# Kernel tuning notes

Measured on AMD Instinct MI355X. Metric: run time of the kernel, lower is better.

The kernel has to match this reference:

```python
import jax, jax.numpy as jnp
import numpy as np
from jax import lax

NUM_IM, ROIS = 32, 128          # images per batch, proposals per image
NUM_CLASSES, EMBED, OBJ_DIM = 151, 200, 2048
HALF_H = 256                    # per-direction LSTM hidden; bi concat -> 512
BN_EPS = 1e-5


def _lstm_dir(xs, wih, whh, b):
    # xs: [T, B, Din] -> hidden states [T, B, H]
    pre = jnp.einsum('tbd,dh->tbh', xs, wih) + b  # precompute input proj
    H = whh.shape[0]
    h0 = jnp.zeros((xs.shape[1], H), xs.dtype)
    def step(carry, pt):
        h, c = carry
        g = pt + h @ whh
        i, f, gg, o = jnp.split(g, 4, axis=-1)
        c = jax.nn.sigmoid(f) * c + jax.nn.sigmoid(i) * jnp.tanh(gg)
        h = jax.nn.sigmoid(o) * jnp.tanh(c)
        return (h, c), h
    _, hs = lax.scan(step, (h0, h0), pre)
    return hs


def _bilstm(x, wih, whh, b):
    # x: [B, T, D] -> [B, T, 2*HALF_H]; wih/whh/b carry both directions on axis 0
    xs = jnp.swapaxes(x, 0, 1)
    fwd = _lstm_dir(xs, wih[0], whh[0], b[0])
    bwd = _lstm_dir(xs[::-1], wih[1], whh[1], b[1])[::-1]
    return jnp.swapaxes(jnp.concatenate([fwd, bwd], -1), 0, 1)


def _context(feats, conf, params):
    # sort_rois: per-image descending confidence order, run 2-layer bi(tree)LSTM,
    # then scatter back with the inverse permutation (as in _sort_by_score).
    D = feats.shape[-1]
    f = feats.reshape(NUM_IM, ROIS, D)
    perm = jnp.argsort(-conf.reshape(NUM_IM, ROIS), axis=1)
    xs = jnp.take_along_axis(f, perm[..., None], axis=1)
    wih0, whh0, b0, wih1, whh1, b1 = params
    h = _bilstm(xs, wih0, whh0, b0)
    h = _bilstm(h, wih1, whh1, b1)
    inv = jnp.argsort(perm, axis=1)
    h = jnp.take_along_axis(h, inv[..., None], axis=1)
    return h.reshape(NUM_IM * ROIS, -1)


def setup_inputs() -> dict:
    key = jax.random.key(0)
    ks = jax.random.split(key, 24)
    N = NUM_IM * ROIS
    obj_fmaps = jax.random.normal(ks[0], (N, OBJ_DIM), jnp.float32)
    obj_logits = jax.random.normal(ks[1], (N, NUM_CLASSES), jnp.float32)
    xy = jax.random.uniform(ks[2], (N, 2), jnp.float32) * 500.0
    wh = jax.random.uniform(ks[3], (N, 2), jnp.float32) * 100.0 + 1.0
    boxes = jnp.concatenate([xy, xy + wh], axis=1)  # valid x1y1x2y2
    im_inds = jnp.repeat(jnp.arange(NUM_IM, dtype=jnp.int64), ROIS)
    w = lambda k, s: (jax.random.normal(k, s, jnp.float32) * 0.02)
    H4 = 4 * HALF_H
    D_obj, D_edge = OBJ_DIM + EMBED + 128, EMBED + 2 * HALF_H + OBJ_DIM
    return {
        'obj_fmaps': obj_fmaps, 'obj_logits': obj_logits, 'boxes': boxes,
        'im_inds': im_inds,
        'obj_embed_w': w(ks[4], (NUM_CLASSES, EMBED)),
        'obj_embed2_w': w(ks[5], (NUM_CLASSES, EMBED)),
        'bn_gamma': jnp.ones((4,), jnp.float32), 'bn_beta': jnp.zeros((4,), jnp.float32),
        'bn_mean': jnp.zeros((4,), jnp.float32), 'bn_var': jnp.ones((4,), jnp.float32),
        'pos_w': w(ks[6], (4, 128)), 'pos_b': jnp.zeros((128,), jnp.float32),
        'obj_wih0': w(ks[7], (2, D_obj, H4)), 'obj_whh0': w(ks[8], (2, HALF_H, H4)),
        'obj_b0': jnp.zeros((2, H4), jnp.float32),
        'obj_wih1': w(ks[9], (2, 2 * HALF_H, H4)), 'obj_whh1': w(ks[10], (2, HALF_H, H4)),
        'obj_b1': jnp.zeros((2, H4), jnp.float32),
        'edge_wih0': w(ks[11], (2, D_edge, H4)), 'edge_whh0': w(ks[12], (2, HALF_H, H4)),
        'edge_b0': jnp.zeros((2, H4), jnp.float32),
        'edge_wih1': w(ks[13], (2, 2 * HALF_H, H4)), 'edge_whh1': w(ks[14], (2, HALF_H, H4)),
        'edge_b1': jnp.zeros((2, H4), jnp.float32),
        'dec_w': w(ks[15], (D_obj + 2 * HALF_H, NUM_CLASSES)),
        'dec_b': jnp.zeros((NUM_CLASSES,), jnp.float32),
    }


def reference(obj_fmaps, obj_logits, boxes, im_inds, obj_embed_w, obj_embed2_w,
              bn_gamma, bn_beta, bn_mean, bn_var, pos_w, pos_b,
              obj_wih0, obj_whh0, obj_b0, obj_wih1, obj_whh1, obj_b1,
              edge_wih0, edge_whh0, edge_b0, edge_wih1, edge_whh1, edge_b1,
              dec_w, dec_b):
    probs = jax.nn.softmax(obj_logits, axis=-1)
    obj_embed = probs @ obj_embed_w                      # soft class embedding
    x1, y1, x2, y2 = boxes[:, 0], boxes[:, 1], boxes[:, 2], boxes[:, 3]
    cs = jnp.stack([(x1 + x2) * 0.5, (y1 + y2) * 0.5, x2 - x1, y2 - y1], axis=-1)
    csn = (cs - bn_mean) * lax.rsqrt(bn_var + BN_EPS) * bn_gamma + bn_beta
    pos = jax.nn.relu(csn @ pos_w + pos_b)               # BN(4)+Linear(4,128)+ReLU
    feats = jnp.concatenate([obj_fmaps, obj_embed, pos], axis=-1)  # [N, 2376]
    conf = jnp.max(probs[:, 1:], axis=-1)                # confidence (non-bg)
    enc = _context(feats, conf, (obj_wih0, obj_whh0, obj_b0,
                                 obj_wih1, obj_whh1, obj_b1))       # [N, 512]
    dec_in = jnp.concatenate([feats, enc], axis=-1)      # pass_in_obj_feats_to_decoder
    obj_dists = dec_in @ dec_w + dec_b                   # [N, 151]
    obj_preds = jnp.argmax(obj_dists[:, 1:], axis=-1) + 1
    edge_in = jnp.concatenate([obj_embed2_w[obj_preds], enc, obj_fmaps], axis=-1)
    edge_ctx = _context(edge_in, conf, (edge_wih0, edge_whh0, edge_b0,
                                        edge_wih1, edge_whh1, edge_b1))  # [N, 512]
    return jnp.concatenate([obj_dists, edge_ctx], axis=-1)  # [N, 663]
```

## Files before the change

kernel.cpp:

```cpp
#include <hip/hip_runtime.h>
#include <hip/hip_bf16.h>
#include <hip/hip_fp16.h>

typedef unsigned short u16;
typedef unsigned int u32;
typedef short s16x8 __attribute__((ext_vector_type(8)));
typedef float f32x4 __attribute__((ext_vector_type(4)));

#define FE_LD 2944
#define EDGE_LD 2816

static __device__ __forceinline__ int sdot4(u32 a, u32 b, int acc) {
  return __builtin_amdgcn_sdot4((int)a, (int)b, acc, false);
}
static __device__ __forceinline__ float fsig(float x) {
  return __builtin_amdgcn_rcpf(1.f + __expf(-x));
}
static __device__ __forceinline__ float ftanh(float x) {
  return 1.f - 2.f * __builtin_amdgcn_rcpf(1.f + __expf(2.f * x));
}

#define GLD_LDS16(gsrc, ldst) \
  __builtin_amdgcn_global_load_lds((const __attribute__((address_space(1))) void*)(gsrc), \
                                   (__attribute__((address_space(3))) void*)(ldst), 16, 0, 0)

__global__ __launch_bounds__(256) void gemm_kernel(
    const u16* __restrict__ A, int lda,
    const u16* __restrict__ B, int ldb,
    int K, int N,
    float* __restrict__ outF, __hip_bfloat16* __restrict__ outB, int ldc,
    const float* __restrict__ bias)
{
  __shared__ __align__(16) u16 As[128*64];
  __shared__ __align__(16) u16 Bs[128*64];
  const int tid = threadIdx.x;
  const int w = tid >> 6, lane = tid & 63;
  const int wm = w >> 1, wn = w & 1;
  const long bm = (long)blockIdx.x * 128;
  const long bn = (long)blockIdx.y * 128;
  f32x4 acc[4][4] = {};

  for (int k0 = 0; k0 < K; k0 += 64) {
    #pragma unroll
    for (int rr = 0; rr < 4; rr++) {
      int idx = rr * 256 + tid;
      int row = idx >> 3;
      int g   = idx & 7;
      int gs  = g ^ (row & 7);
      int ldst = (rr * 256 + (w << 6)) * 8;
      GLD_LDS16(A + (bm + row) * (long)lda + k0 + gs * 8, &As[ldst]);
      GLD_LDS16(B + (bn + row) * (long)ldb + k0 + gs * 8, &Bs[ldst]);
    }
    __syncthreads();
    #pragma unroll
    for (int kk = 0; kk < 2; kk++) {
      s16x8 af[4], bfr[4];
      #pragma unroll
      for (int i = 0; i < 4; i++) {
        int ra = wm * 64 + i * 16 + (lane & 15);
        int rb = wn * 64 + i * 16 + (lane & 15);
        int gg = kk * 4 + (lane >> 4);
        af[i]  = *(const s16x8*)&As[ra * 64 + ((gg ^ (ra & 7)) << 3)];
        bfr[i] = *(const s16x8*)&Bs[rb * 64 + ((gg ^ (rb & 7)) << 3)];
      }
      #pragma unroll
      for (int i = 0; i < 4; i++)
        #pragma unroll
        for (int j = 0; j < 4; j++)
          acc[i][j] = __builtin_amdgcn_mfma_f32_16x16x32_bf16(af[i], bfr[j], acc[i][j], 0, 0, 0);
    }
    __syncthreads();
  }

  #pragma unroll
  for (int i = 0; i < 4; i++)
    #pragma unroll
    for (int j = 0; j < 4; j++)
      #pragma unroll
      for (int v = 0; v < 4; v++) {
        long rr = bm + wm * 64 + i * 16 + (lane >> 4) * 4 + v;
        int  cc = (int)bn + wn * 64 + j * 16 + (lane & 15);
        if (cc < N) {
          float val = acc[i][j][v] + (bias ? bias[cc] : 0.f);
          if (outF) outF[rr * (long)ldc + cc] = val;
          else      outB[rr * (long)ldc + cc] = __float2bfloat16(val);
        }
      }
}

#define N_TROPS 10
struct TrOps {
  const float* src[N_TROPS];
  __hip_bfloat16* dst[N_TROPS];
  int srcK[N_TROPS], srcN[N_TROPS], dstR[N_TROPS], dstC[N_TROPS];
  int split[N_TROPS], soff[N_TROPS];
  int tileBase[N_TROPS], tilesX[N_TROPS];
};
__global__ void transpose_batch(TrOps ops)
{
  __shared__ float tile[32][33];
  int bid = blockIdx.x;
  int op = 0;
  #pragma unroll
  for (int i = 1; i < N_TROPS; i++) if (bid >= ops.tileBase[i]) op = i;
  const int local = bid - ops.tileBase[op];
  const int kt = (local % ops.tilesX[op]) * 32;
  const int nt = (local / ops.tilesX[op]) * 32;
  const float* src = ops.src[op];
  __hip_bfloat16* dst = ops.dst[op];
  const int srcK = ops.srcK[op], srcN = ops.srcN[op];
  const int dstR = ops.dstR[op], dstC = ops.dstC[op];
  const int split = ops.split[op], soff = ops.soff[op];

  const int tx = threadIdx.x & 31, ty = threadIdx.x >> 5;
  for (int i = ty; i < 32; i += 8) {
    int k = kt + i;
    int srck = (k < split) ? (soff + k) : (k - split);
    int n = nt + tx;
    tile[i][tx] = (srck < srcK && n < srcN) ? src[(size_t)srck * srcN + n] : 0.f;
  }
  __syncthreads();
  for (int i = ty; i < 32; i += 8) {
    int n = nt + i, k = kt + tx;
    if (n < dstR && k < dstC)
      dst[(size_t)n * dstC + k] = __float2bfloat16(tile[tx][i]);
  }
}

struct PkOps {
  const float* whh[4];
  u32* wreg[4];
  u32* wlds[4];
  float* wsc[4];
};
__global__ void pack_batch(PkOps ops)
{
  const int set = blockIdx.y;
  const float* whh = ops.whh[set];
  u32* wreg = ops.wreg[set];
  u32* wlds = ops.wlds[set];
  float* wsc = ops.wsc[set];

  const int idx = blockIdx.x * 256 + threadIdx.x;
  const int d = idx >> 10, col = idx & 1023;
  const int c4 = col >> 8, j = col & 255;
  const float* s = whh + (size_t)d * 256 * 1024 + col;
  float mx = 0.f;
  for (int k = 0; k < 256; k++) mx = fmaxf(mx, fabsf(s[(size_t)k * 1024]));
  float inv = (mx > 0.f) ? 127.f / mx : 0.f;
  wsc[d * 1024 + col] = (mx > 0.f) ? mx / (127.f * 127.f) : 0.f;
  const int rc = (c4 < 2) ? 12 : 8;
  const int rb = (c4 == 0) ? 0 : (c4 == 1) ? 12 : (c4 == 2) ? 24 : 32;
  for (int kg = 0; kg < 4; kg++) {
    const int slot = kg * 256 + j;
    for (int w = 0; w < 16; w++) {
      u32 v = 0;
      #pragma unroll
      for (int b = 0; b < 4; b++) {
        int q = __float2int_rn(s[(size_t)(kg * 64 + 4 * w + b) * 1024] * inv);
        q = max(-127, min(127, q));
        v |= ((u32)(q & 0xff)) << (8 * b);
      }
      if (w < rc) {
        wreg[(size_t)(d * 40 + rb + w) * 1024 + slot] = v;
      } else {
        int qq, comp;
        if (c4 == 0)      { qq = 0; comp = w - 12; }
        else if (c4 == 1) { qq = 1; comp = w - 12; }
        else if (c4 == 2) { qq = 2 + ((w - 8) >> 2); comp = (w - 8) & 3; }
        else              { qq = 4 + ((w - 8) >> 2); comp = (w - 8) & 3; }
        wlds[((size_t)(d * 6 + qq) * 1024 + slot) * 4 + comp] = v;
      }
    }
  }
}

__global__ void prep_kernel(
    const float* __restrict__ logits, const float* __restrict__ fmaps,
    const float* __restrict__ boxes,
    const float* __restrict__ bn_g, const float* __restrict__ bn_b,
    const float* __restrict__ bn_m, const float* __restrict__ bn_v,
    const float* __restrict__ pos_w, const float* __restrict__ pos_b,
    __hip_bfloat16* __restrict__ FE, __hip_bfloat16* __restrict__ probsb,
    float* __restrict__ conf)
{
  __shared__ float red[256];
  const int row = blockIdx.x, t = threadIdx.x;
  float v = (t < 151) ? logits[(size_t)row * 151 + t] : -3.0e38f;
  red[t] = v; __syncthreads();
  for (int s = 128; s > 0; s >>= 1) { if (t < s) red[t] = fmaxf(red[t], red[t + s]); __syncthreads(); }
  float mx = red[0]; __syncthreads();
  float p = (t < 151) ? expf(v - mx) : 0.f;
  red[t] = p; __syncthreads();
  for (int s = 128; s > 0; s >>= 1) { if (t < s) red[t] += red[t + s]; __syncthreads(); }
  float sum = red[0]; __syncthreads();
  p = p / sum;
  if (t < 192) probsb[(size_t)row * 192 + t] = __float2bfloat16((t < 151) ? p : 0.f);
  red[t] = (t >= 1 && t < 151) ? p : 0.f; __syncthreads();
  for (int s = 128; s > 0; s >>= 1) { if (t < s) red[t] = fmaxf(red[t], red[t + s]); __syncthreads(); }
  if (t == 0) conf[row] = red[0];

  if (t < 128) {
    float x1 = boxes[row * 4 + 0], y1 = boxes[row * 4 + 1];
    float x2 = boxes[row * 4 + 2], y2 = boxes[row * 4 + 3];
    float cs[4] = { (x1 + x2) * 0.5f, (y1 + y2) * 0.5f, x2 - x1, y2 - y1 };
    float a = pos_b[t];
    #pragma unroll
    for (int j = 0; j < 4; j++) {
      float cn = (cs[j] - bn_m[j]) * rsqrtf(bn_v[j] + 1e-5f) * bn_g[j] + bn_b[j];
      a += cn * pos_w[j * 128 + t];
    }
    FE[(size_t)row * FE_LD + 2760 + t] = __float2bfloat16(fmaxf(a, 0.f));
  }
  for (int c0 = t; c0 < 2048; c0 += 256)
    FE[(size_t)row * FE_LD + 512 + c0] = __float2bfloat16(fmaps[(size_t)row * 2048 + c0]);
}

__global__ void sort_kernel(const float* __restrict__ conf, int* __restrict__ perm)
{
  __shared__ float key[128];
  __shared__ int   idx[128];
  const int b = blockIdx.x, t = threadIdx.x;
  key[t] = conf[b * 128 + t]; idx[t] = t;
  __syncthreads();
  for (int k = 2; k <= 128; k <<= 1)
    for (int j = k >> 1; j > 0; j >>= 1) {
      int ixj = t ^ j;
      if (ixj > t) {
        bool up = (t & k) == 0;
        float ka = key[t], kb = key[ixj];
        int ia = idx[t], ib = idx[ixj];
        bool before = (ka > kb) || (ka == kb && ia < ib);
        if (before != up) { key[t] = kb; key[ixj] = ka; idx[t] = ib; idx[ixj] = ia; }
      }
      __syncthreads();
    }
  perm[b * 128 + t] = b * 128 + idx[t];
}

__global__ __launch_bounds__(1024) void rec_kernel(
    const __hip_bfloat16* __restrict__ P,
    const int* __restrict__ perm,
    const u32* __restrict__ wreg_g,
    const uint4* __restrict__ wlds_g,
    const float* __restrict__ wsc_g,
    int gatherPerm, int outPerm,
    __hip_bfloat16* __restrict__ out_bf, int out_ld,
    float* __restrict__ out_f32, int f32_ld, int f32_off)
{
  __shared__ __align__(16) uint4 wt4[6 * 1024];
  __shared__ __align__(16) int4 part[256 * 5];
  __shared__ __align__(16) u32 hq[64];
  __shared__ int prow_lds[128];
  const int tid = threadIdx.x;
  const int kg = tid >> 8;
  const int img = blockIdx.x & 31, dir = blockIdx.x >> 5;

  u32 wv[40];
  {
    const u32* rp = wreg_g + (size_t)dir * 40960 + tid;
    #pragma unroll
    for (int i = 0; i < 40; i++) wv[i] = rp[(size_t)i * 1024];
  }
  #pragma unroll
  for (int i = 0; i < 40; i++) asm volatile("" : "+v"(wv[i]));
  {
    const uint4* lp = wlds_g + (size_t)dir * 6144 + tid;
    #pragma unroll
    for (int q = 0; q < 6; q++) wt4[q * 1024 + tid] = lp[(size_t)q * 1024];
  }
  if (tid < 128) prow_lds[tid] = perm[img * 128 + tid];
  if (tid < 64) hq[tid] = 0;

  float sc0 = 0.f, sc1 = 0.f, sc2 = 0.f, sc3 = 0.f, cst = 0.f;
  if (tid < 256) {
    const float* sp = wsc_g + dir * 1024 + tid;
    sc0 = sp[0]; sc1 = sp[256]; sc2 = sp[512]; sc3 = sp[768];
  }
  __syncthreads();

  const uint4* hq4 = (const uint4*)hq;

  int st = dir ? 127 : 0;
  float p0 = 0.f, p1 = 0.f, p2 = 0.f, p3 = 0.f;
  if (tid < 256) {
    int prow0 = gatherPerm ? prow_lds[st] : (img * 128 + st);
    const __hip_bfloat16* pp = P + (size_t)prow0 * 2048 + dir * 1024 + tid;
    p0 = __bfloat162float(pp[0]);   p1 = __bfloat162float(pp[256]);
    p2 = __bfloat162float(pp[512]); p3 = __bfloat162float(pp[768]);
  }

  for (int t = 0; t < 128; t++) {
    float n0 = 0.f, n1 = 0.f, n2 = 0.f, n3 = 0.f;
    if (tid < 256 && t < 127) {
      int stn = dir ? (126 - t) : (t + 1);
      int prn = gatherPerm ? prow_lds[stn] : (img * 128 + stn);
      const __hip_bfloat16* pp = P + (size_t)prn * 2048 + dir * 1024 + tid;
      n0 = __bfloat162float(pp[0]);   n1 = __bfloat162float(pp[256]);
      n2 = __bfloat162float(pp[512]); n3 = __bfloat162float(pp[768]);
    }

    int a0 = 0, a1 = 0, a2 = 0, a3 = 0;
    {
      uint4 hv = hq4[kg * 4 + 0];
      a0 = sdot4(hv.x, wv[0], a0);  a0 = sdot4(hv.y, wv[1], a0);
      a0 = sdot4(hv.z, wv[2], a0);  a0 = sdot4(hv.w, wv[3], a0);
      a1 = sdot4(hv.x, wv[12], a1); a1 = sdot4(hv.y, wv[13], a1);
      a1 = sdot4(hv.z, wv[14], a1); a1 = sdot4(hv.w, wv[15], a1);
      a2 = sdot4(hv.x, wv[24], a2); a2 = sdot4(hv.y, wv[25], a2);
      a2 = sdot4(hv.z, wv[26], a2); a2 = sdot4(hv.w, wv[27], a2);
      a3 = sdot4(hv.x, wv[32], a3); a3 = sdot4(hv.y, wv[33], a3);
      a3 = sdot4(hv.z, wv[34], a3); a3 = sdot4(hv.w, wv[35], a3);
    }
    {
      uint4 hv = hq4[kg * 4 + 1];
      a0 = sdot4(hv.x, wv[4], a0);  a0 = sdot4(hv.y, wv[5], a0);
      a0 = sdot4(hv.z, wv[6], a0);  a0 = sdot4(hv.w, wv[7], a0);
      a1 = sdot4(hv.x, wv[16], a1); a1 = sdot4(hv.y, wv[17], a1);
      a1 = sdot4(hv.z, wv[18], a1); a1 = sdot4(hv.w, wv[19], a1);
      a2 = sdot4(hv.x, wv[28], a2); a2 = sdot4(hv.y, wv[29], a2);
      a2 = sdot4(hv.z, wv[30], a2); a2 = sdot4(hv.w, wv[31], a2);
      a3 = sdot4(hv.x, wv[36], a3); a3 = sdot4(hv.y, wv[37], a3);
      a3 = sdot4(hv.z, wv[38], a3); a3 = sdot4(hv.w, wv[39], a3);
    }
    {
      uint4 hv = hq4[kg * 4 + 2];
      a0 = sdot4(hv.x, wv[8], a0);  a0 = sdot4(hv.y, wv[9], a0);
      a0 = sdot4(hv.z, wv[10], a0); a0 = sdot4(hv.w, wv[11], a0);
      a1 = sdot4(hv.x, wv[20], a1); a1 = sdot4(hv.y, wv[21], a1);
      a1 = sdot4(hv.z, wv[22], a1); a1 = sdot4(hv.w, wv[23], a1);
      uint4 wl = wt4[2 * 1024 + tid];
      a2 = sdot4(hv.x, wl.x, a2); a2 = sdot4(hv.y, wl.y, a2);
      a2 = sdot4(hv.z, wl.z, a2); a2 = sdot4(hv.w, wl.w, a2);
      wl = wt4[4 * 1024 + tid];
      a3 = sdot4(hv.x, wl.x, a3); a3 = sdot4(hv.y, wl.y, a3);
      a3 = sdot4(hv.z, wl.z, a3); a3 = sdot4(hv.w, wl.w, a3);
    }
    {
      uint4 hv = hq4[kg * 4 + 3];
      uint4 wl = wt4[0 * 1024 + tid];
      a0 = sdot4(hv.x, wl.x, a0); a0 = sdot4(hv.y, wl.y, a0);
      a0 = sdot4(hv.z, wl.z, a0); a0 = sdot4(hv.w, wl.w, a0);
      wl = wt4[1 * 1024 + tid];
      a1 = sdot4(hv.x, wl.x, a1); a1 = sdot4(hv.y, wl.y, a1);
      a1 = sdot4(hv.z, wl.z, a1); a1 = sdot4(hv.w, wl.w, a1);
      wl = wt4[3 * 1024 + tid];
      a2 = sdot4(hv.x, wl.x, a2); a2 = sdot4(hv.y, wl.y, a2);
      a2 = sdot4(hv.z, wl.z, a2); a2 = sdot4(hv.w, wl.w, a2);
      wl = wt4[5 * 1024 + tid];
      a3 = sdot4(hv.x, wl.x, a3); a3 = sdot4(hv.y, wl.y, a3);
      a3 = sdot4(hv.z, wl.z, a3); a3 = sdot4(hv.w, wl.w, a3);
    }

    part[(tid & 255) * 5 + kg] = int4{a0, a1, a2, a3};
    __syncthreads();

    if (tid < 256) {
      int4 q0 = part[tid * 5 + 0], q1 = part[tid * 5 + 1];
      int4 q2 = part[tid * 5 + 2], q3 = part[tid * 5 + 3];
      float gi = (float)(q0.x + q1.x + q2.x + q3.x) * sc0 + p0;
      float gf = (float)(q0.y + q1.y + q2.y + q3.y) * sc1 + p1;
      float gg = (float)(q0.z + q1.z + q2.z + q3.z) * sc2 + p2;
      float go = (float)(q0.w + q1.w + q2.w + q3.w) * sc3 + p3;
      float si = fsig(gi), sf = fsig(gf), so = fsig(go);
      cst = sf * cst + si * ftanh(gg);
      float h = so * ftanh(cst);
      int qi = __float2int_rn(h * 127.f);
      ((signed char*)hq)[tid] = (signed char)qi;
      const int orow = outPerm ? prow_lds[st] : (img * 128 + st);
      if (out_bf)  out_bf[(size_t)orow * out_ld + dir * 256 + tid] = __float2bfloat16(h);
      if (out_f32) out_f32[(size_t)orow * f32_ld + f32_off + dir * 256 + tid] = h;
    }
    __syncthreads();
    p0 = n0; p1 = n1; p2 = n2; p3 = n3;
    st = dir ? (st - 1) : (st + 1);
  }
}

__global__ void argmax_edge_kernel(const float* __restrict__ dists,
                                   const float* __restrict__ embed2,
                                   const float* __restrict__ fmaps,
                                   const __hip_bfloat16* __restrict__ FE,
                                   __hip_bfloat16* __restrict__ EDGE)
{
  __shared__ float rv[256];
  __shared__ int   ri[256];
  const int row = blockIdx.x, t = threadIdx.x;

  float best = (t < 150) ? dists[(size_t)row * 663 + 1 + t] : -3.4e38f;
  int   bi   = (t < 150) ? (1 + t) : 1000;
  rv[t] = best; ri[t] = bi;
  __syncthreads();
  for (int s = 128; s > 0; s >>= 1) {
    if (t < s) {
      float ov = rv[t + s]; int oi = ri[t + s];
      if (ov > rv[t] || (ov == rv[t] && oi < ri[t])) { rv[t] = ov; ri[t] = oi; }
    }
    __syncthreads();
  }
  const int pr = ri[0];

  for (int c0 = t; c0 < 200; c0 += 256)
    EDGE[(size_t)row * EDGE_LD + c0] = __float2bfloat16(embed2[(size_t)pr * 200 + c0]);
  for (int c0 = t; c0 < 512; c0 += 256)
    EDGE[(size_t)row * EDGE_LD + 200 + c0] = FE[(size_t)row * FE_LD + c0];
  for (int c0 = t; c0 < 2048; c0 += 256)
    EDGE[(size_t)row * EDGE_LD + 712 + c0] = __float2bfloat16(fmaps[(size_t)row * 2048 + c0]);
}

extern "C" void kernel_launch(void* const* d_in, const int* in_sizes, int n_in,
                              void* d_out, int out_size, void* d_ws, size_t ws_size,
                              hipStream_t stream)
{
  const float* obj_fmaps    = (const float*)d_in[0];
  const float* obj_logits   = (const float*)d_in[1];
  const float* boxes        = (const float*)d_in[2];
  const float* obj_embed_w  = (const float*)d_in[4];
  const float* obj_embed2_w = (const float*)d_in[5];
  const float* bn_g = (const float*)d_in[6];
  const float* bn_b = (const float*)d_in[7];
  const float* bn_m = (const float*)d_in[8];
  const float* bn_v = (const float*)d_in[9];
  const float* pos_w = (const float*)d_in[10];
  const float* pos_b = (const float*)d_in[11];
  const float* obj_wih0 = (const float*)d_in[12];
  const float* obj_whh0 = (const float*)d_in[13];
  const float* obj_b0   = (const float*)d_in[14];
  const float* obj_wih1 = (const float*)d_in[15];
  const float* obj_whh1 = (const float*)d_in[16];
  const float* obj_b1   = (const float*)d_in[17];
  const float* edge_wih0 = (const float*)d_in[18];
  const float* edge_whh0 = (const float*)d_in[19];
  const float* edge_b0   = (const float*)d_in[20];
  const float* edge_wih1 = (const float*)d_in[21];
  const float* edge_whh1 = (const float*)d_in[22];
  const float* edge_b1   = (const float*)d_in[23];
  const float* dec_w = (const float*)d_in[24];
  const float* dec_b = (const float*)d_in[25];
  float* out = (float*)d_out;

  char* ws = (char*)d_ws;
  auto alloc = [&](size_t bytes) -> char* {
    char* p = ws; ws += (bytes + 255) & ~(size_t)255; return p;
  };
  __hip_bfloat16* FE     = (__hip_bfloat16*)alloc(4096ull * FE_LD * 2);
  __hip_bfloat16* EDGE   = (__hip_bfloat16*)alloc(4096ull * EDGE_LD * 2);
  __hip_bfloat16* Pbuf   = (__hip_bfloat16*)alloc(4096ull * 2048 * 2);
  __hip_bfloat16* hseq   = (__hip_bfloat16*)alloc(4096ull * 512 * 2);
  __hip_bfloat16* probsb = (__hip_bfloat16*)alloc(4096ull * 192 * 2);
  __hip_bfloat16* wih0T  = (__hip_bfloat16*)alloc(2048ull * 2432 * 2);
  __hip_bfloat16* wih1T  = (__hip_bfloat16*)alloc(2048ull * 512 * 2);
  __hip_bfloat16* ewih0T = (__hip_bfloat16*)alloc(2048ull * 2816 * 2);
  __hip_bfloat16* ewih1T = (__hip_bfloat16*)alloc(2048ull * 512 * 2);
  __hip_bfloat16* embedT = (__hip_bfloat16*)alloc(256ull * 192 * 2);
  __hip_bfloat16* decT   = (__hip_bfloat16*)alloc(256ull * 2944 * 2);
  u32* whh0pk  = (u32*)alloc(133120ull * 4);
  u32* whh1pk  = (u32*)alloc(133120ull * 4);
  u32* ewhh0pk = (u32*)alloc(133120ull * 4);
  u32* ewhh1pk = (u32*)alloc(133120ull * 4);
  int*   perm  = (int*)alloc(4096 * 4);
  float* conf  = (float*)alloc(4096 * 4);
  (void)in_sizes; (void)n_in; (void)out_size; (void)ws_size;

  TrOps tr{};
  int nt = 0, base = 0;
  auto addTr = [&](const float* src, __hip_bfloat16* dst, int srcK, int srcN,
                   int dstR, int dstC, int split, int soff) {
    tr.src[nt] = src; tr.dst[nt] = dst;
    tr.srcK[nt] = srcK; tr.srcN[nt] = srcN; tr.dstR[nt] = dstR; tr.dstC[nt] = dstC;
    tr.split[nt] = split; tr.soff[nt] = soff;
    int tx = (dstC + 31) / 32, ty = (dstR + 31) / 32;
    tr.tileBase[nt] = base; tr.tilesX[nt] = tx;
    base += tx * ty; nt++;
  };
  for (int d = 0; d < 2; d++) {
    addTr(obj_wih0 + (size_t)d * 2376 * 1024, wih0T + (size_t)d * 1024 * 2432, 2376, 1024, 1024, 2432, 0, 0);
    addTr(obj_wih1 + (size_t)d * 512 * 1024,  wih1T + (size_t)d * 1024 * 512,  512, 1024, 1024, 512, 0, 0);
    addTr(edge_wih0 + (size_t)d * 2760 * 1024, ewih0T + (size_t)d * 1024 * 2816, 2760, 1024, 1024, 2816, 0, 0);
    addTr(edge_wih1 + (size_t)d * 512 * 1024,  ewih1T + (size_t)d * 1024 * 512,  512, 1024, 1024, 512, 0, 0);
  }
  addTr(obj_embed_w, embedT, 151, 200, 256, 192, 0, 0);
  addTr(dec_w, decT, 2888, 151, 256, 2944, 512, 2376);
  transpose_batch<<<dim3(base), dim3(256), 0, stream>>>(tr);

  PkOps pk{};
  const float* whhs[4] = {obj_whh0, obj_whh1, edge_whh0, edge_whh1};
  u32* pks[4] = {whh0pk, whh1pk, ewhh0pk, ewhh1pk};
  for (int i = 0; i < 4; i++) {
    pk.whh[i] = whhs[i];
    pk.wreg[i] = pks[i];
    pk.wlds[i] = pks[i] + 81920;
    pk.wsc[i]  = (float*)(pks[i] + 131072);
  }
  pack_batch<<<dim3(8, 4), dim3(256), 0, stream>>>(pk);

  prep_kernel<<<dim3(4096), dim3(256), 0, stream>>>(
      obj_logits, obj_fmaps, boxes, bn_g, bn_b, bn_m, bn_v, pos_w, pos_b, FE, probsb, conf);
  sort_kernel<<<dim3(32), dim3(128), 0, stream>>>(conf, perm);

  auto gemm = [&](const void* A, int lda, const void* B, int ldb, int K, int N,
                  float* oF, __hip_bfloat16* oB, int ldc, const float* bias) {
    dim3 g(32, (N + 127) / 128);
    gemm_kernel<<<g, dim3(256), 0, stream>>>(
        (const u16*)A, lda, (const u16*)B, ldb, K, N, oF, oB, ldc, bias);
  };
  auto rec = [&](const __hip_bfloat16* P, const u32* wpk, int gat, int op,
                 __hip_bfloat16* ob, int old_, float* of, int fld, int foff) {
    rec_kernel<<<dim3(64), dim3(1024), 0, stream>>>(
        P, perm, wpk, (const uint4*)(wpk + 81920), (const float*)(wpk + 131072),
        gat, op, ob, old_, of, fld, foff);
  };

  gemm(probsb, 192, embedT, 192, 192, 200, nullptr, FE + 2560, FE_LD, nullptr);
  gemm((const u16*)FE + 512, FE_LD, wih0T, 2432, 2432, 2048, nullptr, Pbuf, 2048, obj_b0);
  rec(Pbuf, whh0pk, 1, 0, hseq, 512, nullptr, 0, 0);
  gemm(hseq, 512, wih1T, 512, 512, 2048, nullptr, Pbuf, 2048, obj_b1);
  rec(Pbuf, whh1pk, 0, 1, FE, FE_LD, nullptr, 0, 0);
  gemm(FE, FE_LD, decT, 2944, 2944, 151, out, nullptr, 663, dec_b);
  argmax_edge_kernel<<<dim3(4096), dim3(256), 0, stream>>>(
      out, obj_embed2_w, obj_fmaps, FE, EDGE);
  gemm(EDGE, EDGE_LD, ewih0T, 2816, 2816, 2048, nullptr, Pbuf, 2048, edge_b0);
  rec(Pbuf, ewhh0pk, 1, 0, hseq, 512, nullptr, 0, 0);
  gemm(hseq, 512, ewih1T, 512, 512, 2048, nullptr, Pbuf, 2048, edge_b1);
  rec(Pbuf, ewhh1pk, 0, 1, nullptr, 0, out, 663, 151);
}
```

Measured before the change: 869.9 us.

## Quantize large LSTM input projections to int8 MFMA and add XCD-aware block mapping

The two largest input-projection GEMMs (features x wih0 for the object and edge contexts) now quantize activations and weights per row to int8 and run an int8 MFMA kernel with K-tiles of 128, rescaling by the row scales in the epilogue. This halves operand bytes and uses the higher-throughput int8 matrix path, at the cost of extra quantization kernels and a loss of accuracy. All GEMM launches also switch to a 1-D grid remapped so that consecutive tiles land on the same XCD, aiming for better L2 reuse.

New measurement: 864.2 us. No clear change (-0.7%).

```diff
diff --git a/kernel.cpp b/kernel.cpp
--- a/kernel.cpp
+++ b/kernel.cpp
@@ -3,9 +3,11 @@
 #include <hip/hip_fp16.h>
 
 typedef unsigned short u16;
+typedef unsigned char u8;
 typedef unsigned int u32;
 typedef short s16x8 __attribute__((ext_vector_type(8)));
 typedef float f32x4 __attribute__((ext_vector_type(4)));
+typedef int i32x4 __attribute__((ext_vector_type(4)));
 
 #define FE_LD 2944
 #define EDGE_LD 2816
@@ -24,10 +26,17 @@
   __builtin_amdgcn_global_load_lds((const __attribute__((address_space(1))) void*)(gsrc), \
                                    (__attribute__((address_space(3))) void*)(ldst), 16, 0, 0)
 
+static __device__ __forceinline__ void xcd_map(int gy, int* bx, int* by) {
+  int lin = blockIdx.x;
+  int q = gridDim.x >> 3;
+  int wg = (lin & 7) * q + (lin >> 3);
+  *bx = wg / gy; *by = wg % gy;
+}
+
 __global__ __launch_bounds__(256) void gemm_kernel(
     const u16* __restrict__ A, int lda,
     const u16* __restrict__ B, int ldb,
-    int K, int N,
+    int K, int N, int gy,
     float* __restrict__ outF, __hip_bfloat16* __restrict__ outB, int ldc,
     const float* __restrict__ bias)
 {
@@ -36,8 +45,9 @@
   const int tid = threadIdx.x;
   const int w = tid >> 6, lane = tid & 63;
   const int wm = w >> 1, wn = w & 1;
-  const long bm = (long)blockIdx.x * 128;
-  const long bn = (long)blockIdx.y * 128;
+  int bxi, byi; xcd_map(gy, &bxi, &byi);
+  const long bm = (long)bxi * 128;
+  const long bn = (long)byi * 128;
   f32x4 acc[4][4] = {};
 
   for (int k0 = 0; k0 < K; k0 += 64) {
@@ -86,6 +96,101 @@
           else      outB[rr * (long)ldc + cc] = __float2bfloat16(val);
         }
       }
+}
+
+__global__ __launch_bounds__(256) void gemm_i8_kernel(
+    const u8* __restrict__ A, int lda,
+    const u8* __restrict__ B, int ldb,
+    int K, int N, int gy,
+    const float* __restrict__ asc, const float* __restrict__ bsc,
+    __hip_bfloat16* __restrict__ outB, int ldc,
+    const float* __restrict__ bias)
+{
+  __shared__ __align__(16) u8 As[128*128];
+  __shared__ __align__(16) u8 Bs[128*128];
+  const int tid = threadIdx.x;
+  const int w = tid >> 6, lane = tid & 63;
+  const int wm = w >> 1, wn = w & 1;
+  int bxi, byi; xcd_map(gy, &bxi, &byi);
+  const long bm = (long)bxi * 128;
+  const long bn = (long)byi * 128;
+  i32x4 acc[4][4] = {};
+
+  for (int k0 = 0; k0 < K; k0 += 128) {
+    #pragma unroll
+    for (int rr = 0; rr < 4; rr++) {
+      int idx = rr * 256 + tid;
+      int row = idx >> 3;
+      int g   = idx & 7;
+      int gs  = g ^ (row & 7);
+      int ldst = (rr * 256 + (w << 6)) * 16;
+      GLD_LDS16(A + (bm + row) * (long)lda + k0 + gs * 16, &As[ldst]);
+      GLD_LDS16(B + (bn + row) * (long)ldb + k0 + gs * 16, &Bs[ldst]);
+    }
+    __syncthreads();
+    #pragma unroll
+    for (int kk = 0; kk < 2; kk++) {
+      i32x4 af[4], bfr[4];
+      #pragma unroll
+      for (int i = 0; i < 4; i++) {
+        int ra = wm * 64 + i * 16 + (lane & 15);
+        int rb = wn * 64 + i * 16 + (lane & 15);
+        int gg = kk * 4 + (lane >> 4);
+        af[i]  = __builtin_bit_cast(i32x4, *(const uint4*)&As[ra * 128 + ((gg ^ (ra & 7)) << 4)]);
+        bfr[i] = __builtin_bit_cast(i32x4, *(const uint4*)&Bs[rb * 128 + ((gg ^ (rb & 7)) << 4)]);
+      }
+      #pragma unroll
+      for (int i = 0; i < 4; i++)
+        #pragma unroll
+        for (int j = 0; j < 4; j++)
+          acc[i][j] = __builtin_amdgcn_mfma_i32_16x16x64_i8(af[i], bfr[j], acc[i][j], 0, 0, 0);
+    }
+    __syncthreads();
+  }
+
+  #pragma unroll
+  for (int i = 0; i < 4; i++)
+    #pragma unroll
+    for (int j = 0; j < 4; j++)
+      #pragma unroll
+      for (int v = 0; v < 4; v++) {
+        long rr = bm + wm * 64 + i * 16 + (lane >> 4) * 4 + v;
+        int  cc = (int)bn + wn * 64 + j * 16 + (lane & 15);
+        if (cc < N) {
+          float val = (float)acc[i][j][v] * asc[rr] * bsc[cc] + (bias ? bias[cc] : 0.f);
+          outB[rr * (long)ldc + cc] = __float2bfloat16(val);
+        }
+      }
+}
+
+__global__ void quant_rows(const u16* __restrict__ src, long ld, int K,
+                           u8* __restrict__ dst, long dld, float* __restrict__ scale)
+{
+  __shared__ float red[256];
+  const int row = blockIdx.x, t = threadIdx.x;
+  const u16* s = src + (size_t)row * ld;
+  float mx = 0.f;
+  for (int c = t; c < K; c += 256) {
+    u32 u = (u32)s[c] << 16;
+    mx = fmaxf(mx, fabsf(__builtin_bit_cast(float, u)));
+  }
+  red[t] = mx; __syncthreads();
+  for (int st = 128; st > 0; st >>= 1) { if (t < st) red[t] = fmaxf(red[t], red[t + st]); __syncthreads(); }
+  mx = red[0];
+  float inv = (mx > 0.f) ? 127.f / mx : 0.f;
+  if (t == 0) scale[row] = (mx > 0.f) ? mx / 127.f : 0.f;
+  u32* d32 = (u32*)(dst + (size_t)row * dld);
+  for (int wd = t; wd < (K >> 2); wd += 256) {
+    u32 v = 0;
+    #pragma unroll
+    for (int b = 0; b < 4; b++) {
+      u32 u = (u32)s[4 * wd + b] << 16;
+      int q = __float2int_rn(__builtin_bit_cast(float, u) * inv);
+      q = max(-127, min(127, q));
+      v |= ((u32)(q & 0xff)) << (8 * b);
+    }
+    d32[wd] = v;
+  }
 }
 
 #define N_TROPS 10
@@ -458,6 +563,14 @@
   u32* whh1pk  = (u32*)alloc(133120ull * 4);
   u32* ewhh0pk = (u32*)alloc(133120ull * 4);
   u32* ewhh1pk = (u32*)alloc(133120ull * 4);
+  u8*  FEq     = (u8*)alloc(4096ull * 2432);
+  u8*  EDGEq   = (u8*)alloc(4096ull * 2816);
+  u8*  wih0q   = (u8*)alloc(2048ull * 2432);
+  u8*  ewih0q  = (u8*)alloc(2048ull * 2816);
+  float* ascFE   = (float*)alloc(4096 * 4);
+  float* ascEDGE = (float*)alloc(4096 * 4);
+  float* bsc0    = (float*)alloc(2048 * 4);
+  float* bsc1    = (float*)alloc(2048 * 4);
   int*   perm  = (int*)alloc(4096 * 4);
   float* conf  = (float*)alloc(4096 * 4);
   (void)in_sizes; (void)n_in; (void)out_size; (void)ws_size;
@@ -494,15 +607,25 @@
   }
   pack_batch<<<dim3(8, 4), dim3(256), 0, stream>>>(pk);
 
+  quant_rows<<<dim3(2048), dim3(256), 0, stream>>>((const u16*)wih0T, 2432, 2432, wih0q, 2432, bsc0);
+  quant_rows<<<dim3(2048), dim3(256), 0, stream>>>((const u16*)ewih0T, 2816, 2816, ewih0q, 2816, bsc1);
+
   prep_kernel<<<dim3(4096), dim3(256), 0, stream>>>(
       obj_logits, obj_fmaps, boxes, bn_g, bn_b, bn_m, bn_v, pos_w, pos_b, FE, probsb, conf);
   sort_kernel<<<dim3(32), dim3(128), 0, stream>>>(conf, perm);
 
   auto gemm = [&](const void* A, int lda, const void* B, int ldb, int K, int N,
                   float* oF, __hip_bfloat16* oB, int ldc, const float* bias) {
-    dim3 g(32, (N + 127) / 128);
-    gemm_kernel<<<g, dim3(256), 0, stream>>>(
-        (const u16*)A, lda, (const u16*)B, ldb, K, N, oF, oB, ldc, bias);
+    int gy = (N + 127) / 128;
+    gemm_kernel<<<dim3(32 * gy), dim3(256), 0, stream>>>(
+        (const u16*)A, lda, (const u16*)B, ldb, K, N, gy, oF, oB, ldc, bias);
+  };
+  auto gemm_i8 = [&](const u8* A, int lda, const u8* B, int ldb, int K, int N,
+                     const float* asc, const float* bsc,
+                     __hip_bfloat16* oB, int ldc, const float* bias) {
+    int gy = (N + 127) / 128;
+    gemm_i8_kernel<<<dim3(32 * gy), dim3(256), 0, stream>>>(
+        A, lda, B, ldb, K, N, gy, asc, bsc, oB, ldc, bias);
   };
   auto rec = [&](const __hip_bfloat16* P, const u32* wpk, int gat, int op,
                  __hip_bfloat16* ob, int old_, float* of, int fld, int foff) {
@@ -512,14 +635,16 @@
   };
 
   gemm(probsb, 192, embedT, 192, 192, 200, nullptr, FE + 2560, FE_LD, nullptr);
-  gemm((const u16*)FE + 512, FE_LD, wih0T, 2432, 2432, 2048, nullptr, Pbuf, 2048, obj_b0);
+  quant_rows<<<dim3(4096), dim3(256), 0, stream>>>((const u16*)FE + 512, FE_LD, 2432, FEq, 2432, ascFE);
+  gemm_i8(FEq, 2432, wih0q, 2432, 2432, 2048, ascFE, bsc0, Pbuf, 2048, obj_b0);
   rec(Pbuf, whh0pk, 1, 0, hseq, 512, nullptr, 0, 0);
   gemm(hseq, 512, wih1T, 512, 512, 2048, nullptr, Pbuf, 2048, obj_b1);
   rec(Pbuf, whh1pk, 0, 1, FE, FE_LD, nullptr, 0, 0);
   gemm(FE, FE_LD, decT, 2944, 2944, 151, out, nullptr, 663, dec_b);
   argmax_edge_kernel<<<dim3(4096), dim3(256), 0, stream>>>(
       out, obj_embed2_w, obj_fmaps, FE, EDGE);
-  gemm(EDGE, EDGE_LD, ewih0T, 2816, 2816, 2048, nullptr, Pbuf, 2048, edge_b0);
+  quant_rows<<<dim3(4096), dim3(256), 0, stream>>>((const u16*)EDGE, EDGE_LD, 2816, EDGEq, 2816, ascEDGE);
+  gemm_i8(EDGEq, 2816, ewih0q, 2816, 2816, 2048, ascEDGE, bsc1, Pbuf, 2048, edge_b0);
   rec(Pbuf, ewhh0pk, 1, 0, hseq, 512, nullptr, 0, 0);
   gemm(hseq, 512, ewih1T, 512, 512, 2048, nullptr, Pbuf, 2048, edge_b1);
   rec(Pbuf, ewhh1pk, 0, 1, nullptr, 0, out, 663, 151);
```
